# Kernel optimization log

Hardware: AMD Instinct MI355X
Metric: run time of the kernel (lower is better)

The kernel has to match this reference:

```python
import jax, jax.numpy as jnp
import numpy as np

# Fixed LeNet C3 connection table: input channel i feeds these 10 output channels.
CONN = [[0, 4, 5, 6, 9, 10, 11, 12, 14, 15],
        [0, 1, 5, 6, 7, 10, 11, 12, 13, 15],
        [0, 1, 2, 6, 7, 8, 11, 13, 14, 15],
        [1, 2, 3, 6, 7, 8, 9, 12, 14, 15],
        [2, 3, 4, 7, 8, 9, 10, 12, 13, 15],
        [3, 4, 5, 8, 9, 10, 11, 13, 14, 15]]
# Static scatter indices: (out_channel, in_channel) pairs, 60 total.
_ROWS = np.concatenate([np.asarray(l, np.int32) for l in CONN])  # out-channel ids
_COLS = np.repeat(np.arange(6, dtype=np.int32), 10)              # in-channel ids


def setup_inputs() -> dict:
    key = jax.random.key(0)
    k1, k2 = jax.random.split(key)
    x = jax.random.normal(k1, (64, 6, 256, 256), jnp.float32)
    # kaiming-uniform-ish scale for 6*5*5 fan-in
    weight = jax.random.normal(k2, (10, 6, 5, 5), jnp.float32) * 0.1
    bias = jnp.full((1, 16, 1, 1), 0.01, jnp.float32)
    return {"x": x, "weight": weight, "bias": bias}


def reference(x, weight, bias):
    # Fold the per-input-channel loop + scatter-add into one dense [16,6,5,5]
    # kernel with zeros where the connection table is absent. Each iteration i
    # of the original adds conv(x[:,i], weight[j,i]) to out channel CONN[i][j].
    w_flat = weight.transpose(1, 0, 2, 3).reshape(60, 5, 5)  # ordered (i, j)
    w_full = jnp.zeros((16, 6, 5, 5), weight.dtype).at[_ROWS, _COLS].set(w_flat)
    # Bias for channel c is added once per list containing c -> multiply by count.
    counts = jnp.zeros((16,), weight.dtype).at[_ROWS].add(1.0)
    out = jax.lax.conv_general_dilated(
        x, w_full, window_strides=(1, 1), padding='VALID',
        dimension_numbers=('NCHW', 'OIHW', 'NCHW'))
    return out + bias * counts.reshape(1, 16, 1, 1)
```

## Files before the change

kernel.cpp:

```cpp
#include <hip/hip_runtime.h>
#include <hip/hip_fp16.h>

typedef _Float16 f16x8 __attribute__((ext_vector_type(8)));
typedef float f32x4 __attribute__((ext_vector_type(4)));

__device__ constexpr int CONN[6][10] = {
    {0, 4, 5, 6, 9, 10, 11, 12, 14, 15},
    {0, 1, 5, 6, 7, 10, 11, 12, 13, 15},
    {0, 1, 2, 6, 7, 8, 11, 13, 14, 15},
    {1, 2, 3, 6, 7, 8, 9, 12, 14, 15},
    {2, 3, 4, 7, 8, 9, 10, 12, 13, 15},
    {3, 4, 5, 8, 9, 10, 11, 13, 14, 15}};

__device__ constexpr int CNT[16] = {3,3,3,3,3,3,4,4,4,4,4,4,4,4,4,6};

__device__ __forceinline__ f16x8 u4_to_h8(uint4 u) { f16x8 r; __builtin_memcpy(&r, &u, 16); return r; }

__global__ void prep_A(const float* __restrict__ w, unsigned short* __restrict__ Wp) {
    int t = blockIdx.x * 256 + threadIdx.x;
    if (t >= 5120) return;
    int j = t & 7, lane = (t >> 3) & 63, ks = t >> 9;
    int ch = lane & 15, kb = lane >> 4;
    float val = 0.f;
    if (kb < 3 && j < 5) {
        int ii = 2 * kb + (ks >= 5 ? 1 : 0);
        int r  = (ks >= 5) ? ks - 5 : ks;
        for (int jj = 0; jj < 10; ++jj)
            if (CONN[ii][jj] == ch) val = w[jj * 150 + ii * 25 + r * 5 + j];
    }
    __half h = __float2half(val);
    unsigned short u; __builtin_memcpy(&u, &h, 2);
    Wp[t] = u;
}

__global__ __launch_bounds__(256, 4) void c3_mfma(
    const float* __restrict__ x, const unsigned short* __restrict__ Wp,
    const float* __restrict__ bias, float* __restrict__ out)
{
    __shared__ char s_raw[6 * 36 * 152];

    const int tid = threadIdx.x;
    int bid = blockIdx.x;
    int id = (bid & 7) * 288 + (bid >> 3);
    const int bx = id & 3;
    const int by = (id >> 2) % 9;
    const int n  = id / 36;
    const int X0 = bx * 64;
    const int Y0 = by * 30;
    const float* xin = x + (size_t)n * 6 * 65536;

    for (int i = tid; i < 6 * 35 * 18; i += 256) {
        int c4  = i % 18;
        int t   = i / 18;
        int row = t % 35;
        int ch  = t / 35;
        int gr  = Y0 + row; if (gr > 255) gr = 255;
        int gc4 = (X0 >> 2) + c4; if (gc4 > 63) gc4 = 63;
        float4 v = *reinterpret_cast<const float4*>(xin + (size_t)ch * 65536 + gr * 256 + gc4 * 4);
        __half2 lo = __floats2half2_rn(v.x, v.y);
        __half2 hi = __floats2half2_rn(v.z, v.w);
        uint2 u; __builtin_memcpy(&u.x, &lo, 4); __builtin_memcpy(&u.y, &hi, 4);
        *reinterpret_cast<uint2*>(s_raw + (ch * 36 + row) * 152 + c4 * 8) = u;
    }
    __syncthreads();

    const int lane = tid & 63;
    const int wv   = tid >> 6;
    const int nn   = lane & 15;
    const int kb   = lane >> 4;

    f16x8 W[10];
    const uint4* wp4 = reinterpret_cast<const uint4*>(Wp);
    #pragma unroll
    for (int ks = 0; ks < 10; ++ks) W[ks] = u4_to_h8(wp4[ks * 64 + lane]);

    const int iiA = (kb < 3) ? 2 * kb : 0;
    const int winoff = (32 * wv + 2 * nn) & ~7;
    const bool hiSel = (nn & 2) != 0;
    const unsigned shb = (unsigned)((nn & 1) * 16);
    const int rowA0 = iiA * 36 * 152 + winoff;

    auto loadf = [&](int a) -> f16x8 {
        uint2 r0 = *reinterpret_cast<const uint2*>(s_raw + a);
        uint2 r1 = *reinterpret_cast<const uint2*>(s_raw + a + 8);
        uint2 r2 = *reinterpret_cast<const uint2*>(s_raw + a + 16);
        unsigned d0 = r0.x, d1 = r0.y, d2 = r1.x, d3 = r1.y, d4 = r2.x, d5 = r2.y;
        unsigned e0 = hiSel ? d1 : d0;
        unsigned e1 = hiSel ? d2 : d1;
        unsigned e2 = hiSel ? d3 : d2;
        unsigned e3 = hiSel ? d4 : d3;
        unsigned e4 = hiSel ? d5 : d4;
        unsigned o0 = (unsigned)((((unsigned long long)e1 << 32) | e0) >> shb);
        unsigned o1 = (unsigned)((((unsigned long long)e2 << 32) | e1) >> shb);
        unsigned o2 = (unsigned)((((unsigned long long)e3 << 32) | e2) >> shb);
        unsigned o3 = (unsigned)((((unsigned long long)e4 << 32) | e3) >> shb);
        return u4_to_h8(make_uint4(o0, o1, o2, o3));
    };

    f16x8 A0 = loadf(rowA0 + 0 * 152), A1 = loadf(rowA0 + 1 * 152),
          A2 = loadf(rowA0 + 2 * 152), A3 = loadf(rowA0 + 3 * 152),
          A4 = loadf(rowA0 + 4 * 152);
    f16x8 B0 = loadf(rowA0 + 5472 + 0 * 152), B1 = loadf(rowA0 + 5472 + 1 * 152),
          B2 = loadf(rowA0 + 5472 + 2 * 152), B3 = loadf(rowA0 + 5472 + 3 * 152),
          B4 = loadf(rowA0 + 5472 + 4 * 152);
    int aN = rowA0 + 5 * 152;

    const int gx = X0 + wv * 16 + nn;
    const bool xok = gx < 252;
    float bb[4];
    #pragma unroll
    for (int q = 0; q < 4; ++q) {
        int ch = kb * 4 + q;
        bb[q] = bias[ch] * (float)CNT[ch];
    }
    float* const op0 = out + (size_t)n * 16 * 63504 + (size_t)(kb * 4) * 63504 + gx;
    int yoff = Y0 * 252;
    int gy = Y0;

#define PHASE(a0,a1,a2,a3,a4,b0,b1,b2,b3,b4)                                   \
    {                                                                          \
        f32x4 acc = {bb[0], bb[1], bb[2], bb[3]};                              \
        acc = __builtin_amdgcn_mfma_f32_16x16x32_f16(W[0], a0, acc, 0, 0, 0);  \
        acc = __builtin_amdgcn_mfma_f32_16x16x32_f16(W[1], a1, acc, 0, 0, 0);  \
        acc = __builtin_amdgcn_mfma_f32_16x16x32_f16(W[2], a2, acc, 0, 0, 0);  \
        acc = __builtin_amdgcn_mfma_f32_16x16x32_f16(W[3], a3, acc, 0, 0, 0);  \
        acc = __builtin_amdgcn_mfma_f32_16x16x32_f16(W[4], a4, acc, 0, 0, 0);  \
        acc = __builtin_amdgcn_mfma_f32_16x16x32_f16(W[5], b0, acc, 0, 0, 0);  \
        acc = __builtin_amdgcn_mfma_f32_16x16x32_f16(W[6], b1, acc, 0, 0, 0);  \
        acc = __builtin_amdgcn_mfma_f32_16x16x32_f16(W[7], b2, acc, 0, 0, 0);  \
        acc = __builtin_amdgcn_mfma_f32_16x16x32_f16(W[8], b3, acc, 0, 0, 0);  \
        acc = __builtin_amdgcn_mfma_f32_16x16x32_f16(W[9], b4, acc, 0, 0, 0);  \
        if (gy < 252 && xok) {                                                 \
            op0[0 * 63504 + yoff] = acc[0];                                    \
            op0[1 * 63504 + yoff] = acc[1];                                    \
            op0[2 * 63504 + yoff] = acc[2];                                    \
            op0[3 * 63504 + yoff] = acc[3];                                    \
        }                                                                      \
        ++gy; yoff += 252;                                                     \
        a0 = loadf(aN); b0 = loadf(aN + 5472); aN += 152;                      \
    }

    #pragma unroll 1
    for (int g = 0; g < 6; ++g) {
        PHASE(A0, A1, A2, A3, A4, B0, B1, B2, B3, B4)
        PHASE(A1, A2, A3, A4, A0, B1, B2, B3, B4, B0)
        PHASE(A2, A3, A4, A0, A1, B2, B3, B4, B0, B1)
        PHASE(A3, A4, A0, A1, A2, B3, B4, B0, B1, B2)
        PHASE(A4, A0, A1, A2, A3, B4, B0, B1, B2, B3)
    }
#undef PHASE
}

extern "C" void kernel_launch(void* const* d_in, const int* in_sizes, int n_in,
                              void* d_out, int out_size, void* d_ws, size_t ws_size,
                              hipStream_t stream) {
    const float* x    = (const float*)d_in[0];
    const float* w    = (const float*)d_in[1];
    const float* bias = (const float*)d_in[2];
    float* out = (float*)d_out;
    unsigned short* Wp = (unsigned short*)d_ws;

    hipLaunchKernelGGL(prep_A, dim3(20), dim3(256), 0, stream, w, Wp);
    hipLaunchKernelGGL(c3_mfma, dim3(2304), dim3(256), 0, stream, x, Wp, bias, out);
}
```

Before: 131.3 us.

## Split MFMA chain into two accumulators and simplify shared-memory window loads

Each output row's 10-deep dependent MFMA chain is split into two interleaved 5-deep chains (accA with bias, accB for the second input channel), summed before the store. This cuts accumulator dependency stalls. The next-row LDS loads are issued right after the first MFMA pair so they overlap with compute. The shared tile drops its padding row, and loadf now reads five dword-aligned words directly instead of three 8-byte loads plus selects, at the cost of more LDS instructions and possible bank-conflict changes.

```diff
diff --git a/kernel.cpp b/kernel.cpp
--- a/kernel.cpp
+++ b/kernel.cpp
@@ -37,7 +37,7 @@
     const float* __restrict__ x, const unsigned short* __restrict__ Wp,
     const float* __restrict__ bias, float* __restrict__ out)
 {
-    __shared__ char s_raw[6 * 36 * 152];
+    __shared__ char s_raw[6 * 35 * 152];
 
     const int tid = threadIdx.x;
     int bid = blockIdx.x;
@@ -60,10 +60,11 @@
         __half2 lo = __floats2half2_rn(v.x, v.y);
         __half2 hi = __floats2half2_rn(v.z, v.w);
         uint2 u; __builtin_memcpy(&u.x, &lo, 4); __builtin_memcpy(&u.y, &hi, 4);
-        *reinterpret_cast<uint2*>(s_raw + (ch * 36 + row) * 152 + c4 * 8) = u;
+        *reinterpret_cast<uint2*>(s_raw + (ch * 35 + row) * 152 + c4 * 8) = u;
     }
     __syncthreads();
 
+    const unsigned* s_dw = reinterpret_cast<const unsigned*>(s_raw);
     const int lane = tid & 63;
     const int wv   = tid >> 6;
     const int nn   = lane & 15;
@@ -75,21 +76,13 @@
     for (int ks = 0; ks < 10; ++ks) W[ks] = u4_to_h8(wp4[ks * 64 + lane]);
 
     const int iiA = (kb < 3) ? 2 * kb : 0;
-    const int winoff = (32 * wv + 2 * nn) & ~7;
-    const bool hiSel = (nn & 2) != 0;
+    const int dwoff = (32 * wv + 2 * nn) >> 2;
     const unsigned shb = (unsigned)((nn & 1) * 16);
-    const int rowA0 = iiA * 36 * 152 + winoff;
 
-    auto loadf = [&](int a) -> f16x8 {
-        uint2 r0 = *reinterpret_cast<const uint2*>(s_raw + a);
-        uint2 r1 = *reinterpret_cast<const uint2*>(s_raw + a + 8);
-        uint2 r2 = *reinterpret_cast<const uint2*>(s_raw + a + 16);
-        unsigned d0 = r0.x, d1 = r0.y, d2 = r1.x, d3 = r1.y, d4 = r2.x, d5 = r2.y;
-        unsigned e0 = hiSel ? d1 : d0;
-        unsigned e1 = hiSel ? d2 : d1;
-        unsigned e2 = hiSel ? d3 : d2;
-        unsigned e3 = hiSel ? d4 : d3;
-        unsigned e4 = hiSel ? d5 : d4;
+    auto loadf = [&](int dwaddr) -> f16x8 {
+        unsigned e0 = s_dw[dwaddr],     e1 = s_dw[dwaddr + 1],
+                 e2 = s_dw[dwaddr + 2], e3 = s_dw[dwaddr + 3],
+                 e4 = s_dw[dwaddr + 4];
         unsigned o0 = (unsigned)((((unsigned long long)e1 << 32) | e0) >> shb);
         unsigned o1 = (unsigned)((((unsigned long long)e2 << 32) | e1) >> shb);
         unsigned o2 = (unsigned)((((unsigned long long)e3 << 32) | e2) >> shb);
@@ -97,13 +90,14 @@
         return u4_to_h8(make_uint4(o0, o1, o2, o3));
     };
 
-    f16x8 A0 = loadf(rowA0 + 0 * 152), A1 = loadf(rowA0 + 1 * 152),
-          A2 = loadf(rowA0 + 2 * 152), A3 = loadf(rowA0 + 3 * 152),
-          A4 = loadf(rowA0 + 4 * 152);
-    f16x8 B0 = loadf(rowA0 + 5472 + 0 * 152), B1 = loadf(rowA0 + 5472 + 1 * 152),
-          B2 = loadf(rowA0 + 5472 + 2 * 152), B3 = loadf(rowA0 + 5472 + 3 * 152),
-          B4 = loadf(rowA0 + 5472 + 4 * 152);
-    int aN = rowA0 + 5 * 152;
+    const int r0dw = iiA * 35 * 38 + dwoff;
+    f16x8 A0 = loadf(r0dw + 0 * 38), A1 = loadf(r0dw + 1 * 38),
+          A2 = loadf(r0dw + 2 * 38), A3 = loadf(r0dw + 3 * 38),
+          A4 = loadf(r0dw + 4 * 38);
+    f16x8 B0 = loadf(r0dw + 1330 + 0 * 38), B1 = loadf(r0dw + 1330 + 1 * 38),
+          B2 = loadf(r0dw + 1330 + 2 * 38), B3 = loadf(r0dw + 1330 + 3 * 38),
+          B4 = loadf(r0dw + 1330 + 4 * 38);
+    int aN = r0dw + 5 * 38;
 
     const int gx = X0 + wv * 16 + nn;
     const bool xok = gx < 252;
@@ -117,27 +111,29 @@
     int yoff = Y0 * 252;
     int gy = Y0;
 
-#define PHASE(a0,a1,a2,a3,a4,b0,b1,b2,b3,b4)                                   \
-    {                                                                          \
-        f32x4 acc = {bb[0], bb[1], bb[2], bb[3]};                              \
-        acc = __builtin_amdgcn_mfma_f32_16x16x32_f16(W[0], a0, acc, 0, 0, 0);  \
-        acc = __builtin_amdgcn_mfma_f32_16x16x32_f16(W[1], a1, acc, 0, 0, 0);  \
-        acc = __builtin_amdgcn_mfma_f32_16x16x32_f16(W[2], a2, acc, 0, 0, 0);  \
-        acc = __builtin_amdgcn_mfma_f32_16x16x32_f16(W[3], a3, acc, 0, 0, 0);  \
-        acc = __builtin_amdgcn_mfma_f32_16x16x32_f16(W[4], a4, acc, 0, 0, 0);  \
-        acc = __builtin_amdgcn_mfma_f32_16x16x32_f16(W[5], b0, acc, 0, 0, 0);  \
-        acc = __builtin_amdgcn_mfma_f32_16x16x32_f16(W[6], b1, acc, 0, 0, 0);  \
-        acc = __builtin_amdgcn_mfma_f32_16x16x32_f16(W[7], b2, acc, 0, 0, 0);  \
-        acc = __builtin_amdgcn_mfma_f32_16x16x32_f16(W[8], b3, acc, 0, 0, 0);  \
-        acc = __builtin_amdgcn_mfma_f32_16x16x32_f16(W[9], b4, acc, 0, 0, 0);  \
-        if (gy < 252 && xok) {                                                 \
-            op0[0 * 63504 + yoff] = acc[0];                                    \
-            op0[1 * 63504 + yoff] = acc[1];                                    \
-            op0[2 * 63504 + yoff] = acc[2];                                    \
-            op0[3 * 63504 + yoff] = acc[3];                                    \
-        }                                                                      \
-        ++gy; yoff += 252;                                                     \
-        a0 = loadf(aN); b0 = loadf(aN + 5472); aN += 152;                      \
+#define PHASE(a0,a1,a2,a3,a4,b0,b1,b2,b3,b4)                                    \
+    {                                                                           \
+        f32x4 accA = {bb[0], bb[1], bb[2], bb[3]};                              \
+        f32x4 accB = {0.f, 0.f, 0.f, 0.f};                                      \
+        accA = __builtin_amdgcn_mfma_f32_16x16x32_f16(W[0], a0, accA, 0, 0, 0); \
+        accB = __builtin_amdgcn_mfma_f32_16x16x32_f16(W[5], b0, accB, 0, 0, 0); \
+        a0 = loadf(aN); b0 = loadf(aN + 1330); aN += 38;                        \
+        accA = __builtin_amdgcn_mfma_f32_16x16x32_f16(W[1], a1, accA, 0, 0, 0); \
+        accB = __builtin_amdgcn_mfma_f32_16x16x32_f16(W[6], b1, accB, 0, 0, 0); \
+        accA = __builtin_amdgcn_mfma_f32_16x16x32_f16(W[2], a2, accA, 0, 0, 0); \
+        accB = __builtin_amdgcn_mfma_f32_16x16x32_f16(W[7], b2, accB, 0, 0, 0); \
+        accA = __builtin_amdgcn_mfma_f32_16x16x32_f16(W[3], a3, accA, 0, 0, 0); \
+        accB = __builtin_amdgcn_mfma_f32_16x16x32_f16(W[8], b3, accB, 0, 0, 0); \
+        accA = __builtin_amdgcn_mfma_f32_16x16x32_f16(W[4], a4, accA, 0, 0, 0); \
+        accB = __builtin_amdgcn_mfma_f32_16x16x32_f16(W[9], b4, accB, 0, 0, 0); \
+        if (gy < 252 && xok) {                                                  \
+            f32x4 acc = accA + accB;                                            \
+            op0[0 * 63504 + yoff] = acc[0];                                     \
+            op0[1 * 63504 + yoff] = acc[1];                                     \
+            op0[2 * 63504 + yoff] = acc[2];                                     \
+            op0[3 * 63504 + yoff] = acc[3];                                     \
+        }                                                                       \
+        ++gy; yoff += 252;                                                      \
     }
 
     #pragma unroll 1
```

Result: no change. 129.2 us (-1.6%).
